# Performance work log

Hardware: AMD Instinct MI355X
Metric: run time of the kernel (lower is better)

The kernel has to match this reference:

```python
import jax, jax.numpy as jnp
import numpy as np

L, N, C = 1024, 32, 512
EPS = 1e-5

def _linear(y, W, b):
    # torch nn.Linear: y @ W.T + b ; y: (L,N,C), W: (C,C)
    return jnp.einsum('lnc,dc->lnd', y, W) + b

def _bn(y, gamma, beta):
    # training-mode BatchNorm1d over (N, C, L) -> stats per channel over (L, N)
    m = y.mean(axis=(0, 1))
    v = y.var(axis=(0, 1))  # biased variance, as torch uses for normalization
    return (y - m) * jax.lax.rsqrt(v + EPS) * gamma + beta

def _indrnn(y, u):
    # h_t = relu(x_t + u * h_{t-1}), elementwise per-channel recurrence over L
    h0 = jnp.zeros(y.shape[1:], y.dtype)
    def step(h, xt):
        h = jax.nn.relu(xt + u * h)
        return h, h
    _, hs = jax.lax.scan(step, h0, y)
    return hs

def setup_inputs() -> dict:
    key = jax.random.key(0)
    ks = jax.random.split(key, 12)
    s = 1.0 / np.sqrt(C)
    x = jax.random.normal(ks[0], (L, N, C), dtype=jnp.float32)
    W1 = jax.random.uniform(ks[1], (C, C), jnp.float32, -s, s)
    b1 = jax.random.uniform(ks[2], (C,), jnp.float32, -s, s)
    g1 = jnp.ones((C,), jnp.float32)
    be1 = jnp.zeros((C,), jnp.float32)
    u1 = jax.random.uniform(ks[3], (C,), jnp.float32, 0.0, 1.0)
    W2 = jax.random.uniform(ks[4], (C, C), jnp.float32, -s, s)
    b2 = jax.random.uniform(ks[5], (C,), jnp.float32, -s, s)
    g2 = jnp.ones((C,), jnp.float32)
    be2 = jnp.zeros((C,), jnp.float32)
    u2 = jax.random.uniform(ks[6], (C,), jnp.float32, 0.0, 1.0)
    return {"x": x, "W1": W1, "b1": b1, "g1": g1, "be1": be1, "u1": u1,
            "W2": W2, "b2": b2, "g2": g2, "be2": be2, "u2": u2}

def reference(x, W1, b1, g1, be1, u1, W2, b2, g2, be2, u2):
    # linear_first=True branch; dropout=0.0 -> identity
    y = _linear(x, W1, b1)
    y = _bn(y, g1, be1)
    y = _indrnn(y, u1)
    y = _linear(y, W2, b2)
    y = _bn(y, g2, be2)
    y = _indrnn(y, u2)
    return y + x
```

## Files before the change

### kernel.cpp

```cpp
#include <hip/hip_runtime.h>
#include <stdint.h>

#define L_DIM 1024
#define N_DIM 32
#define C_DIM 512
#define M_DIM (L_DIM * N_DIM)
#define EPS_BN 1e-5f

typedef __attribute__((ext_vector_type(8))) short bf16x8;
typedef __attribute__((ext_vector_type(4))) float f32x4;

__device__ __forceinline__ unsigned short f2bf(float f) {
  union { float f; unsigned int u; } a; a.f = f;
  unsigned int u = a.u;
  return (unsigned short)((u + 0x7FFFu + ((u >> 16) & 1u)) >> 16);
}
__device__ __forceinline__ float bf2f(unsigned short h) {
  union { float f; unsigned int u; } a; a.u = ((unsigned int)h) << 16;
  return a.f;
}

__device__ __forceinline__ void gl16(const void* g, void* l) {
  __builtin_amdgcn_global_load_lds(
      (const __attribute__((address_space(1))) unsigned int*)g,
      (__attribute__((address_space(3))) unsigned int*)l, 16, 0, 0);
}

__global__ void k_split_all(const float* __restrict__ x, const float* __restrict__ W1,
                            const float* __restrict__ W2,
                            unsigned short* __restrict__ Ahi,
                            unsigned short* __restrict__ W1hi,
                            unsigned short* __restrict__ W2hi) {
  const int NX = M_DIM * C_DIM / 4;
  const int NW = C_DIM * C_DIM / 4;
  int i = blockIdx.x * 256 + threadIdx.x;
  int stride = gridDim.x * 256;
  for (; i < NX + 2 * NW; i += stride) {
    const float4* src; unsigned short* dh; int j;
    if (i < NX)            { src = (const float4*)x;  dh = Ahi;  j = i; }
    else if (i < NX + NW)  { src = (const float4*)W1; dh = W1hi; j = i - NX; }
    else                   { src = (const float4*)W2; dh = W2hi; j = i - NX - NW; }
    float4 v = src[j];
    ushort4 h;
    h.x = f2bf(v.x); h.y = f2bf(v.y); h.z = f2bf(v.z); h.w = f2bf(v.w);
    ((ushort4*)dh)[j] = h;
  }
}

__global__ __launch_bounds__(512, 2)
void k_gemm(const unsigned short* __restrict__ Ahi,
            const unsigned short* __restrict__ Bhi,
            const float* __restrict__ bias, float* __restrict__ C,
            float* __restrict__ gsum, float* __restrict__ gsq) {
  const int K = C_DIM;
  int d = blockIdx.x;
  int xcd = d & 7;
  int q = d >> 3;
  int bm = xcd * 16 + (q >> 1);
  int bn = q & 1;

  __shared__ unsigned short lds[2][16384];

  int tid  = threadIdx.x;
  int lane = tid & 63;
  int wave = tid >> 6;
  int wm = wave >> 2;
  int wn = wave & 3;
  int lr = lane & 15;
  int lk = lane >> 4;

  f32x4 acc[8][4];
#pragma unroll
  for (int i = 0; i < 8; ++i)
#pragma unroll
    for (int j = 0; j < 4; ++j) acc[i][j] = (f32x4){0.f, 0.f, 0.f, 0.f};

  const int ra0 = tid & 255, ka0 = (tid >> 8) & 3;
  const int ra1 = (tid + 512) & 255, ka1 = ((tid + 512) >> 8) & 3;
  const int oa0 = (bm * 256 + ra0) * K + ka0 * 8;
  const int oa1 = (bm * 256 + ra1) * K + ka1 * 8;
  const int ob0 = (bn * 256 + ra0) * K + ka0 * 8;
  const int ob1 = (bn * 256 + ra1) * K + ka1 * 8;

#define STAGE(buf, kk)                                          \
  do {                                                          \
    unsigned short* Lb = lds[buf];                              \
    gl16(Ahi + oa0 + (kk), Lb + (tid) * 8);                     \
    gl16(Ahi + oa1 + (kk), Lb + (tid + 512) * 8);               \
    gl16(Bhi + ob0 + (kk), Lb + (tid + 1024) * 8);              \
    gl16(Bhi + ob1 + (kk), Lb + (tid + 1536) * 8);              \
  } while (0)

#define COMPUTE(buf)                                                          \
  do {                                                                        \
    const unsigned short* Lb = lds[buf];                                      \
    bf16x8 bh[4], af[8];                                                      \
    _Pragma("unroll")                                                         \
    for (int nj = 0; nj < 4; ++nj) {                                          \
      int slot = lk * 256 + wn * 64 + nj * 16 + lr;                           \
      bh[nj] = *(const bf16x8*)(Lb + 8192 + slot * 8);                        \
    }                                                                         \
    _Pragma("unroll")                                                         \
    for (int mi = 0; mi < 8; ++mi) {                                          \
      int slot = lk * 256 + wm * 128 + mi * 16 + lr;                          \
      af[mi] = *(const bf16x8*)(Lb + slot * 8);                               \
    }                                                                         \
    _Pragma("unroll")                                                         \
    for (int mi = 0; mi < 8; ++mi)                                            \
      _Pragma("unroll")                                                       \
      for (int nj = 0; nj < 4; ++nj)                                          \
        acc[mi][nj] = __builtin_amdgcn_mfma_f32_16x16x32_bf16(af[mi], bh[nj], acc[mi][nj], 0, 0, 0); \
  } while (0)

  const int nt = K >> 5;
  STAGE(0, 0);
  STAGE(1, 32);

  for (int t = 0; t < nt - 1; ++t) {
    asm volatile("s_waitcnt vmcnt(4)" ::: "memory");
    __builtin_amdgcn_sched_barrier(0);
    __builtin_amdgcn_s_barrier();
    COMPUTE(t & 1);
    __builtin_amdgcn_s_barrier();
    if (t < nt - 2) STAGE(t & 1, (t + 2) << 5);
  }
  asm volatile("s_waitcnt vmcnt(0)" ::: "memory");
  __builtin_amdgcn_sched_barrier(0);
  __builtin_amdgcn_s_barrier();
  COMPUTE((nt - 1) & 1);

#pragma unroll
  for (int nj = 0; nj < 4; ++nj) {
    int gn = bn * 256 + wn * 64 + nj * 16 + lr;
    float bv = bias[gn];
    float s = 0.f, qq = 0.f;
#pragma unroll
    for (int mi = 0; mi < 8; ++mi) {
      int gm = bm * 256 + wm * 128 + mi * 16 + (lk << 2);
#pragma unroll
      for (int r = 0; r < 4; ++r) {
        float v = acc[mi][nj][r] + bv;
        C[(gm + r) * C_DIM + gn] = v;
        s += v; qq += v * v;
      }
    }
    s  += __shfl_xor(s, 16);  qq += __shfl_xor(qq, 16);
    s  += __shfl_xor(s, 32);  qq += __shfl_xor(qq, 32);
    if (lk == 0) {
      atomicAdd(&gsum[gn], s);
      atomicAdd(&gsq[gn], qq);
    }
  }
#undef STAGE
#undef COMPUTE
}


__global__ __launch_bounds__(1024, 4)
void k_indrnn_split(const float* __restrict__ y,
                    const float* __restrict__ gsum, const float* __restrict__ gsq,
                    const float* __restrict__ g, const float* __restrict__ be,
                    const float* __restrict__ u,
                    unsigned short* __restrict__ hhi) {
  __shared__ float tA[1024], tB[1024], tM[1024];
  int lane = threadIdx.x & 63;
  int w = threadIdx.x >> 6;
  int chain = blockIdx.x * 64 + lane;
  int c = chain & 511;
  float m  = gsum[c] * (1.0f / (float)M_DIM);
  float vv = gsq[c]  * (1.0f / (float)M_DIM) - m * m;
  float sc = g[c] * rsqrtf(vv + EPS_BN);
  float sh = be[c] - m * sc;
  float uu = u[c];
  const float* py = y + chain;
  const int base = w * 64;

  float A = 0.f, Bc = 1.f, Mx = 0.f;
  for (int c0 = 0; c0 < 64; c0 += 16) {
    float vb[16];
#pragma unroll
    for (int i = 0; i < 16; ++i) vb[i] = py[(base + c0 + i) * 16384];
#pragma unroll
    for (int i = 0; i < 16; ++i) {
      float xt = fmaf(vb[i], sc, sh);
      A  = fmaf(uu, A, xt);
      Mx = fmaxf(fmaf(uu, Mx, xt), 0.f);
      Bc *= uu;
    }
  }
  tA[w * 64 + lane] = A; tB[w * 64 + lane] = Bc; tM[w * 64 + lane] = Mx;
  __syncthreads();

  float pA = 0.f, pM = 0.f;
  for (int s = 0; s < w; ++s) {
    float a = tA[s * 64 + lane], b = tB[s * 64 + lane], mm = tM[s * 64 + lane];
    pA = fmaf(b, pA, a);
    pM = fmaxf(fmaf(b, pM, a), mm);
  }
  float h = fmaxf(pA, pM);

  unsigned short* ph = hhi + chain;
  for (int c0 = 0; c0 < 64; c0 += 16) {
    float vb[16];
#pragma unroll
    for (int i = 0; i < 16; ++i) vb[i] = py[(base + c0 + i) * 16384];
#pragma unroll
    for (int i = 0; i < 16; ++i) {
      float xt = fmaf(vb[i], sc, sh);
      h = fmaxf(fmaf(uu, h, xt), 0.f);
      ph[(base + c0 + i) * 16384] = f2bf(h);
    }
  }
}

__global__ __launch_bounds__(1024, 4)
void k_indrnn_res(float* __restrict__ y, const float* __restrict__ x,
                  const float* __restrict__ gsum, const float* __restrict__ gsq,
                  const float* __restrict__ g, const float* __restrict__ be,
                  const float* __restrict__ u) {
  __shared__ float tA[1024], tB[1024], tM[1024];
  int lane = threadIdx.x & 63;
  int w = threadIdx.x >> 6;
  int chain = blockIdx.x * 64 + lane;
  int c = chain & 511;
  float m  = gsum[c] * (1.0f / (float)M_DIM);
  float vv = gsq[c]  * (1.0f / (float)M_DIM) - m * m;
  float sc = g[c] * rsqrtf(vv + EPS_BN);
  float sh = be[c] - m * sc;
  float uu = u[c];
  float* py = y + chain;
  const float* px = x + chain;
  const int base = w * 64;

  float A = 0.f, Bc = 1.f, Mx = 0.f;
  for (int c0 = 0; c0 < 64; c0 += 16) {
    float vb[16];
#pragma unroll
    for (int i = 0; i < 16; ++i) vb[i] = py[(base + c0 + i) * 16384];
#pragma unroll
    for (int i = 0; i < 16; ++i) {
      float xt = fmaf(vb[i], sc, sh);
      A  = fmaf(uu, A, xt);
      Mx = fmaxf(fmaf(uu, Mx, xt), 0.f);
      Bc *= uu;
    }
  }
  tA[w * 64 + lane] = A; tB[w * 64 + lane] = Bc; tM[w * 64 + lane] = Mx;
  __syncthreads();

  float pA = 0.f, pM = 0.f;
  for (int s = 0; s < w; ++s) {
    float a = tA[s * 64 + lane], b = tB[s * 64 + lane], mm = tM[s * 64 + lane];
    pA = fmaf(b, pA, a);
    pM = fmaxf(fmaf(b, pM, a), mm);
  }
  float h = fmaxf(pA, pM);

  for (int c0 = 0; c0 < 64; c0 += 16) {
    float vb[16], xb[16];
#pragma unroll
    for (int i = 0; i < 16; ++i) vb[i] = py[(base + c0 + i) * 16384];
#pragma unroll
    for (int i = 0; i < 16; ++i) xb[i] = px[(base + c0 + i) * 16384];
#pragma unroll
    for (int i = 0; i < 16; ++i) {
      float xt = fmaf(vb[i], sc, sh);
      h = fmaxf(fmaf(uu, h, xt), 0.f);
      py[(base + c0 + i) * 16384] = h + xb[i];
    }
  }
}

extern "C" void kernel_launch(void* const* d_in, const int* in_sizes, int n_in,
                              void* d_out, int out_size, void* d_ws, size_t ws_size,
                              hipStream_t stream) {
  if (n_in < 11) return;
  const float* x   = (const float*)d_in[0];
  const float* W1  = (const float*)d_in[1];
  const float* b1  = (const float*)d_in[2];
  const float* g1  = (const float*)d_in[3];
  const float* be1 = (const float*)d_in[4];
  const float* u1  = (const float*)d_in[5];
  const float* W2  = (const float*)d_in[6];
  const float* b2  = (const float*)d_in[7];
  const float* g2  = (const float*)d_in[8];
  const float* be2 = (const float*)d_in[9];
  const float* u2  = (const float*)d_in[10];
  float* out = (float*)d_out;

  char* ws = (char*)d_ws;
  const size_t SZ_HALF = (size_t)M_DIM * C_DIM * sizeof(unsigned short);
  const size_t SZ_W    = (size_t)C_DIM * C_DIM * sizeof(unsigned short);
  unsigned short* Ahi  = (unsigned short*)(ws);
  unsigned short* W1hi = (unsigned short*)(ws + SZ_HALF);
  unsigned short* W2hi = W1hi + C_DIM * C_DIM;
  float* stats = (float*)(ws + SZ_HALF + 2 * SZ_W);
  float* sum1 = stats,        *sq1 = stats + 512;
  float* sum2 = stats + 1024, *sq2 = stats + 1536;
  if (ws_size < SZ_HALF + 2 * SZ_W + 4 * 512 * sizeof(float)) return;

  hipMemsetAsync(stats, 0, 4 * 512 * sizeof(float), stream);

  k_split_all<<<2048, 256, 0, stream>>>(x, W1, W2, Ahi, W1hi, W2hi);

  dim3 gemmGrid(256);
  k_gemm<<<gemmGrid, 512, 0, stream>>>(Ahi, W1hi, b1, out, sum1, sq1);
  k_indrnn_split<<<256, 1024, 0, stream>>>(out, sum1, sq1, g1, be1, u1, Ahi);

  k_gemm<<<gemmGrid, 512, 0, stream>>>(Ahi, W2hi, b2, out, sum2, sq2);
  k_indrnn_res<<<256, 1024, 0, stream>>>(out, x, sum2, sq2, g2, be2, u2);
}
```

Before: 169.0 us.

## Store GEMM outputs as bf16 and shrink GEMM tiles to 128x128

The GEMM now writes its biased output in bf16 to a separate workspace buffer instead of fp32, and the IndRNN kernels read bf16 and convert on load. The final kernel writes to the output buffer rather than in place. The GEMM tile also drops from 256x256 with 512 threads to 128x128 with 256 threads over 1024 blocks, which raises occupancy and block count. The aim is to halve the intermediate memory traffic between the GEMM and the recurrence, at the cost of bf16 rounding in the pre-BN activations and more redundant operand loads per output.

```diff
diff --git a/kernel.cpp b/kernel.cpp
--- a/kernel.cpp
+++ b/kernel.cpp
@@ -47,66 +47,65 @@
   }
 }
 
-__global__ __launch_bounds__(512, 2)
-void k_gemm(const unsigned short* __restrict__ Ahi,
-            const unsigned short* __restrict__ Bhi,
-            const float* __restrict__ bias, float* __restrict__ C,
+__global__ __launch_bounds__(256, 4)
+void k_gemm(const unsigned short* __restrict__ A,
+            const unsigned short* __restrict__ B,
+            const float* __restrict__ bias, unsigned short* __restrict__ C,
             float* __restrict__ gsum, float* __restrict__ gsq) {
   const int K = C_DIM;
   int d = blockIdx.x;
   int xcd = d & 7;
   int q = d >> 3;
-  int bm = xcd * 16 + (q >> 1);
-  int bn = q & 1;
-
-  __shared__ unsigned short lds[2][16384];
+  int bm = xcd * 32 + (q >> 2);
+  int bn = q & 3;
+
+  __shared__ unsigned short lds[2][8192];
 
   int tid  = threadIdx.x;
   int lane = tid & 63;
   int wave = tid >> 6;
-  int wm = wave >> 2;
-  int wn = wave & 3;
+  int wm = wave >> 1;
+  int wn = wave & 1;
   int lr = lane & 15;
   int lk = lane >> 4;
 
-  f32x4 acc[8][4];
-#pragma unroll
-  for (int i = 0; i < 8; ++i)
+  f32x4 acc[4][4];
+#pragma unroll
+  for (int i = 0; i < 4; ++i)
 #pragma unroll
     for (int j = 0; j < 4; ++j) acc[i][j] = (f32x4){0.f, 0.f, 0.f, 0.f};
 
-  const int ra0 = tid & 255, ka0 = (tid >> 8) & 3;
-  const int ra1 = (tid + 512) & 255, ka1 = ((tid + 512) >> 8) & 3;
-  const int oa0 = (bm * 256 + ra0) * K + ka0 * 8;
-  const int oa1 = (bm * 256 + ra1) * K + ka1 * 8;
-  const int ob0 = (bn * 256 + ra0) * K + ka0 * 8;
-  const int ob1 = (bn * 256 + ra1) * K + ka1 * 8;
+  const int ra = tid & 127, ka = tid >> 7;
+  const int oa0 = (bm * 128 + ra) * K + ka * 8;
+  const int oa1 = (bm * 128 + ra) * K + (ka + 2) * 8;
+  const int ob0 = (bn * 128 + ra) * K + ka * 8;
+  const int ob1 = (bn * 128 + ra) * K + (ka + 2) * 8;
 
 #define STAGE(buf, kk)                                          \
   do {                                                          \
     unsigned short* Lb = lds[buf];                              \
-    gl16(Ahi + oa0 + (kk), Lb + (tid) * 8);                     \
-    gl16(Ahi + oa1 + (kk), Lb + (tid + 512) * 8);               \
-    gl16(Bhi + ob0 + (kk), Lb + (tid + 1024) * 8);              \
-    gl16(Bhi + ob1 + (kk), Lb + (tid + 1536) * 8);              \
+    gl16(A + oa0 + (kk), Lb + (tid) * 8);                       \
+    gl16(A + oa1 + (kk), Lb + (tid + 256) * 8);                 \
+    gl16(B + ob0 + (kk), Lb + (tid + 512) * 8);                 \
+    gl16(B + ob1 + (kk), Lb + (tid + 768) * 8);                 \
   } while (0)
 
 #define COMPUTE(buf)                                                          \
   do {                                                                        \
     const unsigned short* Lb = lds[buf];                                      \
-    bf16x8 bh[4], af[8];                                                      \
+    bf16x8 bh[4], af[4];                                                      \
     _Pragma("unroll")                                                         \
     for (int nj = 0; nj < 4; ++nj) {                                          \
-      int slot = lk * 256 + wn * 64 + nj * 16 + lr;                           \
-      bh[nj] = *(const bf16x8*)(Lb + 8192 + slot * 8);                        \
+      int slot = 512 + lk * 128 + wn * 64 + nj * 16 + lr;                     \
+      bh[nj] = *(const bf16x8*)(Lb + slot * 8);                               \
     }                                                                         \
     _Pragma("unroll")                                                         \
-    for (int mi = 0; mi < 8; ++mi) {                                          \
-      int slot = lk * 256 + wm * 128 + mi * 16 + lr;                          \
+    for (int mi = 0; mi < 4; ++mi) {                                          \
+      int slot = lk * 128 + wm * 64 + mi * 16 + lr;                           \
       af[mi] = *(const bf16x8*)(Lb + slot * 8);                               \
     }                                                                         \
     _Pragma("unroll")                                                         \
-    for (int mi = 0; mi < 8; ++mi)                                            \
+    for (int mi = 0; mi < 4; ++mi)                                            \
       _Pragma("unroll")                                                       \
       for (int nj = 0; nj < 4; ++nj)                                          \
         acc[mi][nj] = __builtin_amdgcn_mfma_f32_16x16x32_bf16(af[mi], bh[nj], acc[mi][nj], 0, 0, 0); \
@@ -131,16 +130,16 @@
 
 #pragma unroll
   for (int nj = 0; nj < 4; ++nj) {
-    int gn = bn * 256 + wn * 64 + nj * 16 + lr;
+    int gn = bn * 128 + wn * 64 + nj * 16 + lr;
     float bv = bias[gn];
     float s = 0.f, qq = 0.f;
 #pragma unroll
-    for (int mi = 0; mi < 8; ++mi) {
-      int gm = bm * 256 + wm * 128 + mi * 16 + (lk << 2);
+    for (int mi = 0; mi < 4; ++mi) {
+      int gm = bm * 128 + wm * 64 + mi * 16 + (lk << 2);
 #pragma unroll
       for (int r = 0; r < 4; ++r) {
         float v = acc[mi][nj][r] + bv;
-        C[(gm + r) * C_DIM + gn] = v;
+        C[(gm + r) * C_DIM + gn] = f2bf(v);
         s += v; qq += v * v;
       }
     }
@@ -157,7 +156,7 @@
 
 
 __global__ __launch_bounds__(1024, 4)
-void k_indrnn_split(const float* __restrict__ y,
+void k_indrnn_split(const unsigned short* __restrict__ y,
                     const float* __restrict__ gsum, const float* __restrict__ gsq,
                     const float* __restrict__ g, const float* __restrict__ be,
                     const float* __restrict__ u,
@@ -172,14 +171,14 @@
   float sc = g[c] * rsqrtf(vv + EPS_BN);
   float sh = be[c] - m * sc;
   float uu = u[c];
-  const float* py = y + chain;
+  const unsigned short* py = y + chain;
   const int base = w * 64;
 
   float A = 0.f, Bc = 1.f, Mx = 0.f;
   for (int c0 = 0; c0 < 64; c0 += 16) {
     float vb[16];
 #pragma unroll
-    for (int i = 0; i < 16; ++i) vb[i] = py[(base + c0 + i) * 16384];
+    for (int i = 0; i < 16; ++i) vb[i] = bf2f(py[(base + c0 + i) * 16384]);
 #pragma unroll
     for (int i = 0; i < 16; ++i) {
       float xt = fmaf(vb[i], sc, sh);
@@ -203,7 +202,7 @@
   for (int c0 = 0; c0 < 64; c0 += 16) {
     float vb[16];
 #pragma unroll
-    for (int i = 0; i < 16; ++i) vb[i] = py[(base + c0 + i) * 16384];
+    for (int i = 0; i < 16; ++i) vb[i] = bf2f(py[(base + c0 + i) * 16384]);
 #pragma unroll
     for (int i = 0; i < 16; ++i) {
       float xt = fmaf(vb[i], sc, sh);
@@ -214,7 +213,8 @@
 }
 
 __global__ __launch_bounds__(1024, 4)
-void k_indrnn_res(float* __restrict__ y, const float* __restrict__ x,
+void k_indrnn_res(const unsigned short* __restrict__ y, const float* __restrict__ x,
+                  float* __restrict__ outp,
                   const float* __restrict__ gsum, const float* __restrict__ gsq,
                   const float* __restrict__ g, const float* __restrict__ be,
                   const float* __restrict__ u) {
@@ -228,15 +228,16 @@
   float sc = g[c] * rsqrtf(vv + EPS_BN);
   float sh = be[c] - m * sc;
   float uu = u[c];
-  float* py = y + chain;
+  const unsigned short* py = y + chain;
   const float* px = x + chain;
+  float* po = outp + chain;
   const int base = w * 64;
 
   float A = 0.f, Bc = 1.f, Mx = 0.f;
   for (int c0 = 0; c0 < 64; c0 += 16) {
     float vb[16];
 #pragma unroll
-    for (int i = 0; i < 16; ++i) vb[i] = py[(base + c0 + i) * 16384];
+    for (int i = 0; i < 16; ++i) vb[i] = bf2f(py[(base + c0 + i) * 16384]);
 #pragma unroll
     for (int i = 0; i < 16; ++i) {
       float xt = fmaf(vb[i], sc, sh);
@@ -259,14 +260,14 @@
   for (int c0 = 0; c0 < 64; c0 += 16) {
     float vb[16], xb[16];
 #pragma unroll
-    for (int i = 0; i < 16; ++i) vb[i] = py[(base + c0 + i) * 16384];
+    for (int i = 0; i < 16; ++i) vb[i] = bf2f(py[(base + c0 + i) * 16384]);
 #pragma unroll
     for (int i = 0; i < 16; ++i) xb[i] = px[(base + c0 + i) * 16384];
 #pragma unroll
     for (int i = 0; i < 16; ++i) {
       float xt = fmaf(vb[i], sc, sh);
       h = fmaxf(fmaf(uu, h, xt), 0.f);
-      py[(base + c0 + i) * 16384] = h + xb[i];
+      po[(base + c0 + i) * 16384] = h + xb[i];
     }
   }
 }
@@ -292,21 +293,22 @@
   const size_t SZ_HALF = (size_t)M_DIM * C_DIM * sizeof(unsigned short);
   const size_t SZ_W    = (size_t)C_DIM * C_DIM * sizeof(unsigned short);
   unsigned short* Ahi  = (unsigned short*)(ws);
-  unsigned short* W1hi = (unsigned short*)(ws + SZ_HALF);
+  unsigned short* Cbf  = (unsigned short*)(ws + SZ_HALF);
+  unsigned short* W1hi = (unsigned short*)(ws + 2 * SZ_HALF);
   unsigned short* W2hi = W1hi + C_DIM * C_DIM;
-  float* stats = (float*)(ws + SZ_HALF + 2 * SZ_W);
+  float* stats = (float*)(ws + 2 * SZ_HALF + 2 * SZ_W);
   float* sum1 = stats,        *sq1 = stats + 512;
   float* sum2 = stats + 1024, *sq2 = stats + 1536;
-  if (ws_size < SZ_HALF + 2 * SZ_W + 4 * 512 * sizeof(float)) return;
+  if (ws_size < 2 * SZ_HALF + 2 * SZ_W + 4 * 512 * sizeof(float)) return;
 
   hipMemsetAsync(stats, 0, 4 * 512 * sizeof(float), stream);
 
   k_split_all<<<2048, 256, 0, stream>>>(x, W1, W2, Ahi, W1hi, W2hi);
 
-  dim3 gemmGrid(256);
-  k_gemm<<<gemmGrid, 512, 0, stream>>>(Ahi, W1hi, b1, out, sum1, sq1);
-  k_indrnn_split<<<256, 1024, 0, stream>>>(out, sum1, sq1, g1, be1, u1, Ahi);
-
-  k_gemm<<<gemmGrid, 512, 0, stream>>>(Ahi, W2hi, b2, out, sum2, sq2);
-  k_indrnn_res<<<256, 1024, 0, stream>>>(out, x, sum2, sq2, g2, be2, u2);
-}
+  dim3 gemmGrid(1024);
+  k_gemm<<<gemmGrid, 256, 0, stream>>>(Ahi, W1hi, b1, Cbf, sum1, sq1);
+  k_indrnn_split<<<256, 1024, 0, stream>>>(Cbf, sum1, sq1, g1, be1, u1, Ahi);
+
+  k_gemm<<<gemmGrid, 256, 0, stream>>>(Ahi, W2hi, b2, Cbf, sum2, sq2);
+  k_indrnn_res<<<256, 1024, 0, stream>>>(Cbf, x, out, sum2, sq2, g2, be2, u2);
+}
```

Result: faster. 158.5 us (-6.2%).
